# Optimization experiments

Hardware: AMD Instinct MI355X
Metric: run time of the kernel (lower is better)

## Reference

```python
import jax, jax.numpy as jnp
import numpy as np

H = 4096          # hidden_size
NH = 32           # num query heads
NKV = 8           # num kv heads
HD = H // NH      # head_dim = 128
GROUPS = NH // NKV
ROPE_BASE = 100000.0
B, S = 1, 2048


def setup_inputs() -> dict:
    key = jax.random.key(0)
    k1, k2, k3 = jax.random.split(key, 3)
    hidden_states = jax.random.normal(k1, (B, S, H), dtype=jnp.float32)
    position_ids = jnp.broadcast_to(jnp.arange(S, dtype=jnp.int32), (B, S))
    op_size = NH * HD + 2 * NKV * HD  # 6144
    w_qkv = jax.random.normal(k2, (op_size, H), dtype=jnp.float32) * 0.02
    w_o = jax.random.normal(k3, (H, H), dtype=jnp.float32) * 0.02
    return {"hidden_states": hidden_states, "position_ids": position_ids,
            "w_qkv": w_qkv, "w_o": w_o}


def _rotate_half(x):
    x1, x2 = x[..., : HD // 2], x[..., HD // 2 :]
    return jnp.concatenate((-x2, x1), axis=-1)


def _rope_cos_sin(position_ids, dtype):
    # inv_freq: [HD/2]
    inv_freq = 1.0 / (ROPE_BASE ** (jnp.arange(0, HD, 2, dtype=jnp.float32) / HD))
    freqs = position_ids.astype(jnp.float32)[..., None] * inv_freq  # [B,S,HD/2]
    emb = jnp.concatenate((freqs, freqs), axis=-1)                  # [B,S,HD]
    return jnp.cos(emb).astype(dtype), jnp.sin(emb).astype(dtype)


def reference(hidden_states, position_ids, w_qkv, w_o):
    b, s, _ = hidden_states.shape
    qkv = jnp.einsum('bsh,oh->bso', hidden_states, w_qkv)
    q_end = NH * HD
    k_end = q_end + NKV * HD
    q = qkv[..., :q_end].reshape(b, s, NH, HD)
    k = qkv[..., q_end:k_end].reshape(b, s, NKV, HD)
    v = qkv[..., k_end:].reshape(b, s, NKV, HD)

    cos, sin = _rope_cos_sin(position_ids, hidden_states.dtype)  # [B,S,HD]
    cos, sin = cos[:, :, None, :], sin[:, :, None, :]            # broadcast over heads
    q = q * cos + _rotate_half(q) * sin
    k = k * cos + _rotate_half(k) * sin

    # GQA: repeat kv heads
    k = jnp.repeat(k, GROUPS, axis=2)  # [B,S,NH,HD]
    v = jnp.repeat(v, GROUPS, axis=2)

    scale = 1.0 / jnp.sqrt(jnp.asarray(HD, dtype=q.dtype))
    scores = jnp.einsum('bqhd,bkhd->bhqk', q, k) * scale  # [B,NH,S,S]
    causal = jnp.tril(jnp.ones((s, s), dtype=bool))
    scores = jnp.where(causal[None, None], scores, jnp.finfo(scores.dtype).min)
    probs = jax.nn.softmax(scores, axis=-1)
    attn = jnp.einsum('bhqk,bkhd->bqhd', probs, v).reshape(b, s, H)
    return jnp.einsum('bsh,oh->bso', attn, w_o)
```

## Files before the change

### kernel.cpp

```cpp
#include <hip/hip_runtime.h>

#define SEQ     2048
#define HDIM    4096
#define NHEADS  32
#define NKVH    8
#define HEADD   128
#define QKV_LD  6144
#define K_OFF   4096
#define V_OFF   5120

typedef __bf16 bf16x8 __attribute__((ext_vector_type(8)));
typedef float  f32x4  __attribute__((ext_vector_type(4)));

__device__ inline float bf2f(unsigned short u) {
  return __uint_as_float(((unsigned int)u) << 16);
}
__device__ inline unsigned short f2bf(float f) {
  unsigned int u = __float_as_uint(f);
  u += 0x7fff + ((u >> 16) & 1);
  return (unsigned short)(u >> 16);
}
__device__ inline unsigned int pack2bf(float a, float b) {
  return (unsigned int)f2bf(a) | ((unsigned int)f2bf(b) << 16);
}

__global__ __launch_bounds__(256) void cvt_bf16(
    const float* __restrict__ s, unsigned short* __restrict__ d, int n8) {
  int i = blockIdx.x * 256 + threadIdx.x;
  int stride = gridDim.x * 256;
  for (; i < n8; i += stride) {
    const float* p = s + (size_t)i * 8;
    float4 x = *(const float4*)p;
    float4 y = *(const float4*)(p + 4);
    uint4 pk;
    pk.x = pack2bf(x.x, x.y);
    pk.y = pack2bf(x.z, x.w);
    pk.z = pack2bf(y.x, y.y);
    pk.w = pack2bf(y.z, y.w);
    *(uint4*)(d + (size_t)i * 8) = pk;
  }
}

template<int A_BF16, int B_BF16, int C_F32>
__global__ __launch_bounds__(256, 2) void gemm_bt(
    const void* __restrict__ Av,
    const void* __restrict__ Bv,
    void* __restrict__ Cv,
    int K, int lda, int ldb, int ldc) {
  __shared__ __align__(16) unsigned short sA[128][64];
  __shared__ __align__(16) unsigned short sB[128][64];

  const int t    = threadIdx.x;
  const int wave = t >> 6;
  const int lane = t & 63;
  const int lrow = lane & 15;
  const int kgrp = lane >> 4;
  const int wm   = (wave >> 1) * 64;
  const int wn   = (wave & 1) * 64;
  const int m0   = blockIdx.x * 128;
  const int n0   = blockIdx.y * 128;

  f32x4 acc[4][4];
  #pragma unroll
  for (int i = 0; i < 4; ++i)
    #pragma unroll
    for (int j = 0; j < 4; ++j)
      #pragma unroll
      for (int e = 0; e < 4; ++e) acc[i][j][e] = 0.f;

  for (int k0 = 0; k0 < K; k0 += 64) {
    __syncthreads();
    if constexpr (A_BF16) {
      #pragma unroll
      for (int c = 0; c < 4; ++c) {
        int chunk = wave * 4 + c;
        int row   = chunk * 8 + (lane >> 3);
        int cg    = (lane & 7) ^ ((lane >> 3) & 7);
        __builtin_amdgcn_global_load_lds(
            (const __attribute__((address_space(1))) unsigned int*)
                ((const unsigned short*)Av + (size_t)(m0 + row) * lda + k0 + cg * 8),
            (__attribute__((address_space(3))) unsigned int*)&sA[chunk * 8][0],
            16, 0, 0);
      }
    } else {
      #pragma unroll
      for (int r = 0; r < 4; ++r) {
        int row = r * 32 + (t >> 3);
        int cg  = t & 7;
        const float* p = (const float*)Av + (size_t)(m0 + row) * lda + k0 + cg * 8;
        float4 x = *(const float4*)p;
        float4 y = *(const float4*)(p + 4);
        uint4 pk;
        pk.x = pack2bf(x.x, x.y);
        pk.y = pack2bf(x.z, x.w);
        pk.z = pack2bf(y.x, y.y);
        pk.w = pack2bf(y.z, y.w);
        *(uint4*)&sA[row][(cg ^ (row & 7)) * 8] = pk;
      }
    }
    if constexpr (B_BF16) {
      #pragma unroll
      for (int c = 0; c < 4; ++c) {
        int chunk = wave * 4 + c;
        int row   = chunk * 8 + (lane >> 3);
        int cg    = (lane & 7) ^ ((lane >> 3) & 7);
        __builtin_amdgcn_global_load_lds(
            (const __attribute__((address_space(1))) unsigned int*)
                ((const unsigned short*)Bv + (size_t)(n0 + row) * ldb + k0 + cg * 8),
            (__attribute__((address_space(3))) unsigned int*)&sB[chunk * 8][0],
            16, 0, 0);
      }
    } else {
      #pragma unroll
      for (int r = 0; r < 4; ++r) {
        int row = r * 32 + (t >> 3);
        int cg  = t & 7;
        const float* p = (const float*)Bv + (size_t)(n0 + row) * ldb + k0 + cg * 8;
        float4 x = *(const float4*)p;
        float4 y = *(const float4*)(p + 4);
        uint4 pk;
        pk.x = pack2bf(x.x, x.y);
        pk.y = pack2bf(x.z, x.w);
        pk.z = pack2bf(y.x, y.y);
        pk.w = pack2bf(y.z, y.w);
        *(uint4*)&sB[row][(cg ^ (row & 7)) * 8] = pk;
      }
    }
    __syncthreads();

    #pragma unroll
    for (int ks = 0; ks < 2; ++ks) {
      bf16x8 af[4], bfm[4];
      #pragma unroll
      for (int i = 0; i < 4; ++i)
        af[i] = *(const bf16x8*)&sA[wm + i*16 + lrow][((ks*4 + kgrp) ^ (lrow & 7)) * 8];
      #pragma unroll
      for (int j = 0; j < 4; ++j)
        bfm[j] = *(const bf16x8*)&sB[wn + j*16 + lrow][((ks*4 + kgrp) ^ (lrow & 7)) * 8];
      #pragma unroll
      for (int i = 0; i < 4; ++i)
        #pragma unroll
        for (int j = 0; j < 4; ++j)
          acc[i][j] = __builtin_amdgcn_mfma_f32_16x16x32_bf16(af[i], bfm[j], acc[i][j], 0, 0, 0);
    }
  }

  #pragma unroll
  for (int i = 0; i < 4; ++i) {
    #pragma unroll
    for (int r = 0; r < 4; ++r) {
      int row = m0 + wm + i*16 + kgrp*4 + r;
      #pragma unroll
      for (int j = 0; j < 4; ++j) {
        int col = n0 + wn + j*16 + lrow;
        if constexpr (C_F32)
          ((float*)Cv)[(size_t)row * ldc + col] = acc[i][j][r];
        else
          ((unsigned short*)Cv)[(size_t)row * ldc + col] = f2bf(acc[i][j][r]);
      }
    }
  }
}

__global__ __launch_bounds__(256) void rope_kernel(
    unsigned short* __restrict__ qkv, const int* __restrict__ pos) {
  int tid  = blockIdx.x * 256 + threadIdx.x;
  int d    = tid & 63;
  int rh   = tid >> 6;
  int head = rh % 40;
  int s    = rh / 40;
  if (s >= SEQ) return;
  unsigned short* p = qkv + (size_t)s * QKV_LD + head * 128 + d;
  float x1 = bf2f(p[0]);
  float x2 = bf2f(p[64]);
  float inv = __expf((float)d * -0.17988946039016608f);
  float ang = (float)pos[s] * inv;
  float sn, c;
  sincosf(ang, &sn, &c);
  p[0]  = f2bf(x1 * c - x2 * sn);
  p[64] = f2bf(x2 * c + x1 * sn);
}

__global__ __launch_bounds__(256, 2) void attn_fwd(
    unsigned short* __restrict__ qkv) {
  __shared__ __align__(16) unsigned short sK[64][136];
  __shared__ __align__(16) unsigned short sVt[128][72];
  __shared__ __align__(16) unsigned short sP[64][72];

  const int t    = threadIdx.x;
  const int wave = t >> 6;
  const int lane = t & 63;
  const int lrow = lane & 15;
  const int kgrp = lane >> 4;
  const int q0   = blockIdx.x * 64;
  const int h    = blockIdx.y;
  const int kvh  = h >> 2;

  bf16x8 qf[4];
  {
    const unsigned short* qrow =
        qkv + (size_t)(q0 + wave*16 + lrow) * QKV_LD + h * HEADD;
    #pragma unroll
    for (int ks = 0; ks < 4; ++ks)
      qf[ks] = *(const bf16x8*)(qrow + ks*32 + kgrp*8);
  }

  f32x4 of[8];
  #pragma unroll
  for (int tt = 0; tt < 8; ++tt)
    #pragma unroll
    for (int e = 0; e < 4; ++e) of[tt][e] = 0.f;
  float m_i[4], l_i[4];
  #pragma unroll
  for (int r = 0; r < 4; ++r) { m_i[r] = -1e30f; l_i[r] = 0.f; }

  const float scale = 0.08838834764831845f;

  for (int k0 = 0; k0 <= q0; k0 += 64) {
    __syncthreads();
    {
      int krow = t >> 4;
      int kcol = (t & 15) * 8;
      #pragma unroll
      for (int r = 0; r < 4; ++r)
        *(uint4*)&sK[r*16 + krow][kcol] =
            *(const uint4*)(qkv + (size_t)(k0 + r*16 + krow) * QKV_LD + K_OFF + kvh*HEADD + kcol);
      int vrow = t & 15;
      int vcol = (t >> 4) * 8;
      #pragma unroll
      for (int r = 0; r < 4; ++r) {
        uint4 v = *(const uint4*)(qkv + (size_t)(k0 + r*16 + vrow) * QKV_LD + V_OFF + kvh*HEADD + vcol);
        const unsigned short* pv = (const unsigned short*)&v;
        #pragma unroll
        for (int j = 0; j < 8; ++j)
          sVt[vcol + j][r*16 + vrow] = pv[j];
      }
    }
    __syncthreads();

    f32x4 st[4];
    #pragma unroll
    for (int tn = 0; tn < 4; ++tn)
      #pragma unroll
      for (int e = 0; e < 4; ++e) st[tn][e] = 0.f;
    #pragma unroll
    for (int ks = 0; ks < 4; ++ks)
      #pragma unroll
      for (int tn = 0; tn < 4; ++tn) {
        bf16x8 kb = *(const bf16x8*)&sK[tn*16 + lrow][ks*32 + kgrp*8];
        st[tn] = __builtin_amdgcn_mfma_f32_16x16x32_bf16(qf[ks], kb, st[tn], 0, 0, 0);
      }

    float mrow[4];
    #pragma unroll
    for (int r = 0; r < 4; ++r) mrow[r] = -1e30f;
    const int qrow_base = q0 + wave*16 + kgrp*4;
    #pragma unroll
    for (int tn = 0; tn < 4; ++tn) {
      int kcol = k0 + tn*16 + lrow;
      #pragma unroll
      for (int r = 0; r < 4; ++r) {
        float s = st[tn][r] * scale;
        if (kcol > qrow_base + r) s = -1e30f;
        st[tn][r] = s;
        mrow[r] = fmaxf(mrow[r], s);
      }
    }
    #pragma unroll
    for (int r = 0; r < 4; ++r)
      #pragma unroll
      for (int off = 1; off < 16; off <<= 1)
        mrow[r] = fmaxf(mrow[r], __shfl_xor(mrow[r], off, 16));

    float alpha[4];
    #pragma unroll
    for (int r = 0; r < 4; ++r) {
      float mnew = fmaxf(m_i[r], mrow[r]);
      alpha[r] = __expf(m_i[r] - mnew);
      m_i[r] = mnew;
    }

    float rsum[4] = {0.f, 0.f, 0.f, 0.f};
    #pragma unroll
    for (int tn = 0; tn < 4; ++tn)
      #pragma unroll
      for (int r = 0; r < 4; ++r) {
        float pr = __expf(st[tn][r] - m_i[r]);
        rsum[r] += pr;
        sP[wave*16 + kgrp*4 + r][tn*16 + lrow] = f2bf(pr);
      }
    #pragma unroll
    for (int r = 0; r < 4; ++r) {
      #pragma unroll
      for (int off = 1; off < 16; off <<= 1)
        rsum[r] += __shfl_xor(rsum[r], off, 16);
      l_i[r] = l_i[r] * alpha[r] + rsum[r];
    }
    #pragma unroll
    for (int tt = 0; tt < 8; ++tt)
      #pragma unroll
      for (int r = 0; r < 4; ++r)
        of[tt][r] *= alpha[r];

    __syncthreads();

    #pragma unroll
    for (int ks = 0; ks < 2; ++ks) {
      bf16x8 pa = *(const bf16x8*)&sP[wave*16 + lrow][ks*32 + kgrp*8];
      #pragma unroll
      for (int tt = 0; tt < 8; ++tt) {
        bf16x8 vb = *(const bf16x8*)&sVt[tt*16 + lrow][ks*32 + kgrp*8];
        of[tt] = __builtin_amdgcn_mfma_f32_16x16x32_bf16(pa, vb, of[tt], 0, 0, 0);
      }
    }
  }

  #pragma unroll
  for (int r = 0; r < 4; ++r) {
    int row = q0 + wave*16 + kgrp*4 + r;
    float inv = 1.f / l_i[r];
    #pragma unroll
    for (int tt = 0; tt < 8; ++tt)
      qkv[(size_t)row * QKV_LD + h*HEADD + tt*16 + lrow] = f2bf(of[tt][r] * inv);
  }
}

extern "C" void kernel_launch(void* const* d_in, const int* in_sizes, int n_in,
                              void* d_out, int out_size, void* d_ws, size_t ws_size,
                              hipStream_t stream) {
  const float* hs    = (const float*)d_in[0];
  const int*   pos   = (const int*)d_in[1];
  const float* w_qkv = (const float*)d_in[2];
  const float* w_o   = (const float*)d_in[3];
  float*       out   = (float*)d_out;

  const size_t N_QKV  = (size_t)SEQ * QKV_LD;
  const size_t N_HS   = (size_t)SEQ * HDIM;
  const size_t N_WQKV = (size_t)QKV_LD * HDIM;
  const size_t N_WO   = (size_t)HDIM * HDIM;

  unsigned short* qkv = (unsigned short*)d_ws;

  const size_t full_ws = (N_QKV + N_HS + N_WQKV + N_WO) * 2;

  if (ws_size >= full_ws) {
    unsigned short* hs_b   = qkv + N_QKV;
    unsigned short* wqkv_b = hs_b + N_HS;
    unsigned short* wo_b   = wqkv_b + N_WQKV;

    cvt_bf16<<<2048, 256, 0, stream>>>(hs,    hs_b,   (int)(N_HS   / 8));
    cvt_bf16<<<2048, 256, 0, stream>>>(w_qkv, wqkv_b, (int)(N_WQKV / 8));
    cvt_bf16<<<2048, 256, 0, stream>>>(w_o,   wo_b,   (int)(N_WO   / 8));

    gemm_bt<1, 1, 0><<<dim3(SEQ/128, QKV_LD/128), 256, 0, stream>>>(
        hs_b, wqkv_b, qkv, HDIM, HDIM, HDIM, QKV_LD);
    rope_kernel<<<(SEQ * 40 * 64) / 256, 256, 0, stream>>>(qkv, pos);
    attn_fwd<<<dim3(SEQ/64, NHEADS), 256, 0, stream>>>(qkv);
    gemm_bt<1, 1, 1><<<dim3(SEQ/128, HDIM/128), 256, 0, stream>>>(
        qkv, wo_b, out, HDIM, QKV_LD, HDIM, HDIM);
  } else {
    gemm_bt<0, 0, 0><<<dim3(SEQ/128, QKV_LD/128), 256, 0, stream>>>(
        hs, w_qkv, qkv, HDIM, HDIM, HDIM, QKV_LD);
    rope_kernel<<<(SEQ * 40 * 64) / 256, 256, 0, stream>>>(qkv, pos);
    attn_fwd<<<dim3(SEQ/64, NHEADS), 256, 0, stream>>>(qkv);
    gemm_bt<1, 0, 1><<<dim3(SEQ/128, HDIM/128), 256, 0, stream>>>(
        qkv, w_o, out, HDIM, QKV_LD, HDIM, HDIM);
  }
}
```

Before: 610.0 us.

## Pair causal query tiles per block and pre-transpose V for async LDS loads

Adds a kernel that transposes V into a separate buffer (reusing the freed hidden-state bf16 area), then replaces the attention kernel with one that processes a low and a high query tile per block. The two tiles share each K/V tile load, which balances causal work across blocks and halves the grid. K and V^T are loaded straight into swizzled LDS with global_load_lds instead of going through registers. The cost is an extra transpose pass plus higher register pressure from carrying two accumulator sets.

```diff
diff --git a/kernel.cpp b/kernel.cpp
--- a/kernel.cpp
+++ b/kernel.cpp
@@ -181,6 +181,211 @@
   p[64] = f2bf(x2 * c + x1 * sn);
 }
 
+__global__ __launch_bounds__(256) void transpose_v(
+    const unsigned short* __restrict__ qkv, unsigned short* __restrict__ vT) {
+  __shared__ unsigned short tile[64][72];
+  const int t  = threadIdx.x;
+  const int s0 = blockIdx.x * 64;
+  const int c0 = blockIdx.y * 64;
+  const int r  = t >> 3;
+  const int cg = (t & 7) * 8;
+  #pragma unroll
+  for (int rr = 0; rr < 2; ++rr) {
+    int row = rr * 32 + r;
+    *(uint4*)&tile[row][cg] =
+        *(const uint4*)(qkv + (size_t)(s0 + row) * QKV_LD + V_OFF + c0 + cg);
+  }
+  __syncthreads();
+  #pragma unroll
+  for (int rr = 0; rr < 2; ++rr) {
+    int c = rr * 32 + r;
+    unsigned short v[8];
+    #pragma unroll
+    for (int j = 0; j < 8; ++j) v[j] = tile[cg + j][c];
+    *(uint4*)(vT + (size_t)(c0 + c) * SEQ + s0 + cg) = *(uint4*)v;
+  }
+}
+
+__device__ __forceinline__ void qk_softmax_tile(
+    const bf16x8* qf, const unsigned short (*sK)[128],
+    unsigned short (*sP)[72],
+    f32x4* of, float* m_i, float* l_i,
+    int lane, int wave, int dq) {
+  const int lrow = lane & 15;
+  const int kgrp = lane >> 4;
+  f32x4 st[4];
+  #pragma unroll
+  for (int tn = 0; tn < 4; ++tn)
+    #pragma unroll
+    for (int e = 0; e < 4; ++e) st[tn][e] = 0.f;
+  #pragma unroll
+  for (int ks = 0; ks < 4; ++ks) {
+    #pragma unroll
+    for (int tn = 0; tn < 4; ++tn) {
+      int cgr = ks * 4 + kgrp;
+      const bf16x8 kb = *(const bf16x8*)
+          &sK[tn*16 + lrow][((cgr & 8) | ((cgr & 7) ^ (lrow & 7))) * 8];
+      st[tn] = __builtin_amdgcn_mfma_f32_16x16x32_bf16(qf[ks], kb, st[tn], 0, 0, 0);
+    }
+  }
+  const float scale2 = 0.12751743f;
+  float mrow[4] = {-1e30f, -1e30f, -1e30f, -1e30f};
+  #pragma unroll
+  for (int tn = 0; tn < 4; ++tn) {
+    #pragma unroll
+    for (int r = 0; r < 4; ++r) {
+      float s = st[tn][r] * scale2;
+      if (tn*16 + lrow > dq + r) s = -1e30f;
+      st[tn][r] = s;
+      mrow[r] = fmaxf(mrow[r], s);
+    }
+  }
+  #pragma unroll
+  for (int r = 0; r < 4; ++r)
+    #pragma unroll
+    for (int off = 1; off < 16; off <<= 1)
+      mrow[r] = fmaxf(mrow[r], __shfl_xor(mrow[r], off, 16));
+  float alpha[4];
+  #pragma unroll
+  for (int r = 0; r < 4; ++r) {
+    float mnew = fmaxf(m_i[r], mrow[r]);
+    alpha[r] = exp2f(m_i[r] - mnew);
+    m_i[r] = mnew;
+  }
+  float rsum[4] = {0.f, 0.f, 0.f, 0.f};
+  #pragma unroll
+  for (int tn = 0; tn < 4; ++tn)
+    #pragma unroll
+    for (int r = 0; r < 4; ++r) {
+      float pr = exp2f(st[tn][r] - m_i[r]);
+      rsum[r] += pr;
+      sP[wave*16 + kgrp*4 + r][tn*16 + lrow] = f2bf(pr);
+    }
+  #pragma unroll
+  for (int r = 0; r < 4; ++r) {
+    #pragma unroll
+    for (int off = 1; off < 16; off <<= 1)
+      rsum[r] += __shfl_xor(rsum[r], off, 16);
+    l_i[r] = l_i[r] * alpha[r] + rsum[r];
+  }
+  #pragma unroll
+  for (int tt = 0; tt < 8; ++tt)
+    #pragma unroll
+    for (int r = 0; r < 4; ++r)
+      of[tt][r] *= alpha[r];
+}
+
+__device__ __forceinline__ void pv_tile(
+    const unsigned short (*sP)[72], const unsigned short (*sVt)[64],
+    f32x4* of, int lane, int wave) {
+  const int lrow = lane & 15;
+  const int kgrp = lane >> 4;
+  #pragma unroll
+  for (int ks = 0; ks < 2; ++ks) {
+    const bf16x8 pa = *(const bf16x8*)&sP[wave*16 + lrow][ks*32 + kgrp*8];
+    #pragma unroll
+    for (int tt = 0; tt < 8; ++tt) {
+      int cgr = ks * 4 + kgrp;
+      const bf16x8 vb = *(const bf16x8*)
+          &sVt[tt*16 + lrow][(cgr ^ (lrow & 7)) * 8];
+      of[tt] = __builtin_amdgcn_mfma_f32_16x16x32_bf16(pa, vb, of[tt], 0, 0, 0);
+    }
+  }
+}
+
+__global__ __launch_bounds__(256, 2) void attn_fwd2(
+    unsigned short* __restrict__ qkv, const unsigned short* __restrict__ vT) {
+  __shared__ __align__(16) unsigned short sK[64][128];
+  __shared__ __align__(16) unsigned short sVt[128][64];
+  __shared__ __align__(16) unsigned short sP[128][72];
+
+  const int t    = threadIdx.x;
+  const int wave = t >> 6;
+  const int lane = t & 63;
+  const int lrow = lane & 15;
+  const int kgrp = lane >> 4;
+  const int p    = blockIdx.x;
+  const int h    = blockIdx.y;
+  const int kvh  = h >> 2;
+  const int qLo  = p * 64;
+  const int qHi  = (31 - p) * 64;
+  const int nTiles = 32 - p;
+  const int nDual  = p + 1;
+
+  bf16x8 qfH[4], qfL[4];
+  {
+    const unsigned short* qr =
+        qkv + (size_t)(qHi + wave*16 + lrow) * QKV_LD + h * HEADD;
+    #pragma unroll
+    for (int ks = 0; ks < 4; ++ks) qfH[ks] = *(const bf16x8*)(qr + ks*32 + kgrp*8);
+    qr = qkv + (size_t)(qLo + wave*16 + lrow) * QKV_LD + h * HEADD;
+    #pragma unroll
+    for (int ks = 0; ks < 4; ++ks) qfL[ks] = *(const bf16x8*)(qr + ks*32 + kgrp*8);
+  }
+
+  f32x4 ofH[8], ofL[8];
+  float mH[4], lH[4], mL[4], lL[4];
+  #pragma unroll
+  for (int tt = 0; tt < 8; ++tt)
+    #pragma unroll
+    for (int e = 0; e < 4; ++e) { ofH[tt][e] = 0.f; ofL[tt][e] = 0.f; }
+  #pragma unroll
+  for (int r = 0; r < 4; ++r) { mH[r] = -1e30f; lH[r] = 0.f; mL[r] = -1e30f; lL[r] = 0.f; }
+
+  for (int kt = 0; kt < nTiles; ++kt) {
+    const int k0 = kt * 64;
+    __syncthreads();
+    #pragma unroll
+    for (int c = 0; c < 4; ++c) {
+      int cc   = wave * 4 + c;
+      int grow = cc * 4 + (lane >> 4);
+      int slot = lane & 15;
+      int cg   = (slot & 8) | ((slot & 7) ^ (grow & 7));
+      __builtin_amdgcn_global_load_lds(
+          (const __attribute__((address_space(1))) unsigned int*)
+              (qkv + (size_t)(k0 + grow) * QKV_LD + K_OFF + kvh*HEADD + cg*8),
+          (__attribute__((address_space(3))) unsigned int*)&sK[cc*4][0],
+          16, 0, 0);
+    }
+    #pragma unroll
+    for (int c = 0; c < 4; ++c) {
+      int cc   = wave * 4 + c;
+      int grow = cc * 8 + (lane >> 3);
+      int slot = lane & 7;
+      int cg   = slot ^ (grow & 7);
+      __builtin_amdgcn_global_load_lds(
+          (const __attribute__((address_space(1))) unsigned int*)
+              (vT + (size_t)(kvh*HEADD + grow) * SEQ + k0 + cg*8),
+          (__attribute__((address_space(3))) unsigned int*)&sVt[cc*8][0],
+          16, 0, 0);
+    }
+    __syncthreads();
+
+    const bool dual = (kt < nDual);
+    qk_softmax_tile(qfH, sK, &sP[0],  ofH, mH, lH, lane, wave,
+                    qHi + wave*16 + kgrp*4 - k0);
+    if (dual)
+      qk_softmax_tile(qfL, sK, &sP[64], ofL, mL, lL, lane, wave,
+                      qLo + wave*16 + kgrp*4 - k0);
+    __syncthreads();
+    pv_tile(&sP[0], sVt, ofH, lane, wave);
+    if (dual) pv_tile(&sP[64], sVt, ofL, lane, wave);
+  }
+
+  #pragma unroll
+  for (int r = 0; r < 4; ++r) {
+    float invH = 1.f / lH[r];
+    float invL = 1.f / lL[r];
+    int rowH = qHi + wave*16 + kgrp*4 + r;
+    int rowL = qLo + wave*16 + kgrp*4 + r;
+    #pragma unroll
+    for (int tt = 0; tt < 8; ++tt) {
+      qkv[(size_t)rowH * QKV_LD + h*HEADD + tt*16 + lrow] = f2bf(ofH[tt][r] * invH);
+      qkv[(size_t)rowL * QKV_LD + h*HEADD + tt*16 + lrow] = f2bf(ofL[tt][r] * invL);
+    }
+  }
+}
+
 __global__ __launch_bounds__(256, 2) void attn_fwd(
     unsigned short* __restrict__ qkv) {
   __shared__ __align__(16) unsigned short sK[64][136];
@@ -347,6 +552,7 @@
     unsigned short* hs_b   = qkv + N_QKV;
     unsigned short* wqkv_b = hs_b + N_HS;
     unsigned short* wo_b   = wqkv_b + N_WQKV;
+    unsigned short* vT     = hs_b;
 
     cvt_bf16<<<2048, 256, 0, stream>>>(hs,    hs_b,   (int)(N_HS   / 8));
     cvt_bf16<<<2048, 256, 0, stream>>>(w_qkv, wqkv_b, (int)(N_WQKV / 8));
@@ -355,7 +561,8 @@
     gemm_bt<1, 1, 0><<<dim3(SEQ/128, QKV_LD/128), 256, 0, stream>>>(
         hs_b, wqkv_b, qkv, HDIM, HDIM, HDIM, QKV_LD);
     rope_kernel<<<(SEQ * 40 * 64) / 256, 256, 0, stream>>>(qkv, pos);
-    attn_fwd<<<dim3(SEQ/64, NHEADS), 256, 0, stream>>>(qkv);
+    transpose_v<<<dim3(SEQ/64, (NKVH*HEADD)/64), 256, 0, stream>>>(qkv, vT);
+    attn_fwd2<<<dim3(16, NHEADS), 256, 0, stream>>>(qkv, vT);
     gemm_bt<1, 1, 1><<<dim3(SEQ/128, HDIM/128), 256, 0, stream>>>(
         qkv, wo_b, out, HDIM, QKV_LD, HDIM, HDIM);
   } else {
```

Measured after the change: 537.1 us. -11.9%, faster.
